# Kernel tuning notes

Hardware: AMD Instinct MI355X
Metric: run time of the kernel (lower is better)

The kernel has to match this reference:

```python
import jax, jax.numpy as jnp
import numpy as np
from jax import lax

MAX_T = 1.0
MAX_Z = float(np.e)  # exp(MAX_T)
BITS = 8


def weight_quantization(w):
    # tanh -> scale by max-abs (no grad through alpha) -> clamp -> round with STE
    w = jnp.tanh(w)
    alpha = lax.stop_gradient(jnp.max(jnp.abs(w)))
    q = 2 ** (BITS - 1) - 1
    w = jnp.clip(w / alpha, -1.0, 1.0) * q
    w = w + lax.stop_gradient(jnp.round(w) - w)
    return w * alpha / q


def t_linear_c(inp, W, max_spike_time):
    # inp: [B, L, Fin], W: [Fout, Fin] -> out: [B, L, Fout]
    idx = jnp.argsort(inp, axis=-1)                              # [B,L,Fin]
    s_inp = jnp.take_along_axis(inp, idx, axis=-1)[..., None]    # [B,L,Fin,1]
    w_sorted = W.T[idx]                                          # [B,L,Fin,Fout]
    w_sorted = weight_quantization(w_sorted)
    mul = s_inp * w_sorted
    w_sum = jnp.cumsum(w_sorted, axis=-2)
    iw_sum = jnp.cumsum(mul, axis=-2)
    out_all = iw_sum / jnp.clip(w_sum - 1.0, 1e-10, 1e10)
    o = jnp.where(w_sum < 1.0, max_spike_time, out_all)
    o = jnp.where(o < s_inp, max_spike_time, o)
    nxt = jnp.concatenate([s_inp[:, :, 1:, :], jnp.ones_like(s_inp[:, :, :1, :])], axis=2)
    o = jnp.where(o > nxt, max_spike_time, o)
    return jnp.min(o, axis=-2)


def t_linear(inp, W, max_spike_time):
    # inp: [B, Fin], W: [Fout, Fin] -> out: [B, Fout]
    idx = jnp.argsort(inp, axis=-1)
    s_inp = jnp.take_along_axis(inp, idx, axis=-1)[..., None]    # [B,Fin,1]
    w_sorted = W.T[idx]                                          # [B,Fin,Fout]
    mul = s_inp * w_sorted
    w_sum = jnp.cumsum(w_sorted, axis=1)
    iw_sum = jnp.cumsum(mul, axis=1)
    out_all = iw_sum / jnp.clip(w_sum - 1.0, 1e-10, 1e10)
    o = jnp.where(w_sum < 1.0, max_spike_time, out_all)
    o = jnp.where(o < s_inp, max_spike_time, o)
    nxt = jnp.concatenate([s_inp[:, 1:, :], jnp.ones_like(s_inp[:, :1, :])], axis=1)
    o = jnp.where(o >= nxt, max_spike_time, o)  # note: >= in t_Linear (vs > in t_Linear_c)
    return jnp.min(o, axis=1)


def unfold(x, k, p, s):
    # torch F.unfold: zero-pad, extract kxk patches; feature order (C, kh, kw)
    B, C, H, W = x.shape
    xp = jnp.pad(x, ((0, 0), (0, 0), (p, p), (p, p)))
    oh = (H + 2 * p - k) // s + 1
    ow = (W + 2 * p - k) // s + 1
    ri = (jnp.arange(oh) * s)[:, None] + jnp.arange(k)           # [oh,k]
    ci = (jnp.arange(ow) * s)[:, None] + jnp.arange(k)           # [ow,k]
    pt = xp[:, :, ri[:, None, :, None], ci[None, :, None, :]]    # [B,C,oh,ow,k,k]
    pt = pt.transpose(0, 2, 3, 1, 4, 5).reshape(B, oh * ow, C * k * k)
    return pt, oh, ow


def t_conv(x, W, k, pad, stride, max_spike_time):
    B = x.shape[0]
    patches, oh, ow = unfold(x, k, pad, stride)                  # [B,L,C*k*k]
    patches = jnp.where(patches < 0.1, max_spike_time, patches)
    out = t_linear_c(patches, W, max_spike_time)                 # [B,L,Cout]
    return out.transpose(0, 2, 1).reshape(B, W.shape[0], oh, ow)


def max_pool2(x):
    return lax.reduce_window(x, -jnp.inf, lax.max, (1, 1, 2, 2), (1, 1, 2, 2), 'VALID')


def min_pool3(x):
    # -MaxPool3x3(stride 2)(-ConstantPad2d(1, 1e5)(x))
    xp = jnp.pad(x, ((0, 0), (0, 0), (1, 1), (1, 1)), constant_values=1e5)
    return -lax.reduce_window(-xp, -jnp.inf, lax.max, (1, 1, 3, 3), (1, 1, 2, 2), 'VALID')


def setup_inputs() -> dict:
    key = jax.random.key(0)
    ks = jax.random.split(key, 8)
    B = 8
    inp = jax.random.normal(ks[0], (B, 1, 64, 64), dtype=jnp.float32)
    conv1_w = jax.random.normal(ks[1], (32, 1, 5, 5), dtype=jnp.float32) * (1.0 / 5.0)
    bn_g = jnp.ones((32,), jnp.float32)
    bn_b = jnp.zeros((32,), jnp.float32)
    bn_m = jnp.zeros((32,), jnp.float32)
    bn_v = jnp.ones((32,), jnp.float32)
    def uw(k, fout, fin):
        return jax.random.uniform(k, (fout, fin), jnp.float32, 0.0, 10.0 / fin)
    w2 = uw(ks[2], 32, 3 * 3 * 32)
    w3 = uw(ks[3], 32, 3 * 3 * 32)
    w4 = uw(ks[4], 64, 3 * 3 * 32)
    w5 = uw(ks[5], 64, 3 * 3 * 64)
    w_fc = uw(ks[6], 10, 8 * 8 * 64)
    return {"inp": inp, "conv1_w": conv1_w, "bn_g": bn_g, "bn_b": bn_b,
            "bn_m": bn_m, "bn_v": bn_v, "w2": w2, "w3": w3, "w4": w4,
            "w5": w5, "w_fc": w_fc}


def reference(inp, conv1_w, bn_g, bn_b, bn_m, bn_v, w2, w3, w4, w5, w_fc):
    x = lax.conv_general_dilated(inp, conv1_w, (1, 1), ((2, 2), (2, 2)),
                                 dimension_numbers=('NCHW', 'OIHW', 'NCHW'))
    x = (x - bn_m[None, :, None, None]) * (bn_g / jnp.sqrt(bn_v + 1e-5))[None, :, None, None] \
        + bn_b[None, :, None, None]
    x = jax.nn.relu(x)
    x = max_pool2(x)                       # [B,32,32,32]
    x = jnp.minimum(x, MAX_T)
    z1 = jnp.exp(x)
    z2 = t_conv(z1, w2, 3, 1, 2, MAX_Z)    # [B,32,16,16]
    z3 = t_conv(z2, w3, 3, 1, 1, MAX_Z)    # [B,32,16,16]
    z3c = z3 * min_pool3(z1)
    z4 = t_conv(z3c, w4, 3, 1, 2, MAX_Z * 2)  # [B,64,8,8]
    z5 = t_conv(z4, w5, 3, 1, 1, MAX_Z * 2)   # [B,64,8,8]
    pm = min_pool3(z3c)                       # [B,32,8,8]
    pm = jnp.concatenate([pm, pm], axis=1)    # [B,64,8,8]
    z5c = (z5 * pm).reshape(z5.shape[0], -1)  # [B,4096]
    return t_linear(z5c, w_fc, MAX_Z * 4)     # [B,10]
```

## Files before the change

kernel.cpp:

```cpp
#include <hip/hip_runtime.h>
#include <hip/hip_bf16.h>
#include <math.h>

#define E32 2.7182817459106445f

__device__ __forceinline__ unsigned long long packkey(float vf, int idx) {
  unsigned u = __float_as_uint(vf);
  u = (u & 0x80000000u) ? ~u : (u | 0x80000000u);
  return (((unsigned long long)u) << 32) | (unsigned)idx;
}
__device__ __forceinline__ float unpackval(unsigned long long k) {
  unsigned m = (unsigned)(k >> 32);
  m = (m & 0x80000000u) ? (m ^ 0x80000000u) : ~m;
  return __uint_as_float(m);
}

__global__ __launch_bounds__(256) void pre1_kernel(
    const float* __restrict__ w2, const float* __restrict__ w3,
    const float* __restrict__ w4, const float* __restrict__ w5,
    float* __restrict__ tanhbuf, float* __restrict__ partials,
    const float* __restrict__ inp, const float* __restrict__ w1,
    const float* __restrict__ g, const float* __restrict__ bb,
    const float* __restrict__ m, const float* __restrict__ vv,
    float* __restrict__ z1) {
  int blk = blockIdx.x;
  if (blk < 288) {
    const float* w; int base_blk, tbase;
    if (blk < 36)       { w = w2; base_blk = 0;   tbase = 0; }
    else if (blk < 72)  { w = w3; base_blk = 36;  tbase = 9216; }
    else if (blk < 144) { w = w4; base_blk = 72;  tbase = 18432; }
    else                { w = w5; base_blk = 144; tbase = 36864; }
    int i = (blk - base_blk) * 256 + threadIdx.x;
    float t = tanhf(w[i]);
    tanhbuf[tbase + i] = t;
    __shared__ float red[256];
    red[threadIdx.x] = fabsf(t);
    __syncthreads();
    for (int s = 128; s > 0; s >>= 1) {
      if (threadIdx.x < s) red[threadIdx.x] = fmaxf(red[threadIdx.x], red[threadIdx.x + s]);
      __syncthreads();
    }
    if (threadIdx.x == 0) partials[blk] = red[0];
    return;
  }
  int idx = (blk - 288) * 256 + threadIdx.x;
  if (idx >= 8 * 32 * 32 * 32) return;
  int x = idx & 31, y = (idx >> 5) & 31, c = (idx >> 10) & 31, b = idx >> 15;
  float scale = g[c] / sqrtf(vv[c] + 1e-5f);
  float bias = bb[c];
  float mean = m[c];
  float mx = -3.402823466e38f;
  for (int dy = 0; dy < 2; ++dy) {
    for (int dx = 0; dx < 2; ++dx) {
      int oy = 2 * y + dy, ox = 2 * x + dx;
      float acc = 0.0f;
      for (int kh = 0; kh < 5; ++kh) {
        int r = oy + kh - 2;
        if (r < 0 || r >= 64) continue;
        for (int kw = 0; kw < 5; ++kw) {
          int cc2 = ox + kw - 2;
          if (cc2 < 0 || cc2 >= 64) continue;
          acc += w1[c * 25 + kh * 5 + kw] * inp[(b * 64 + r) * 64 + cc2];
        }
      }
      float xs = (acc - mean) * scale + bias;
      xs = fmaxf(xs, 0.0f);
      mx = fmaxf(mx, xs);
    }
  }
  mx = fminf(mx, 1.0f);
  z1[idx] = (mx == 1.0f) ? E32 : expf(mx);
}

__global__ __launch_bounds__(256) void pre2_kernel(
    const float* __restrict__ tanhbuf, const float* __restrict__ partials,
    float* __restrict__ q2, float* __restrict__ q3,
    float* __restrict__ q4, float* __restrict__ q5,
    const float* __restrict__ wfc, float* __restrict__ wfcT,
    const float* __restrict__ z1, float* __restrict__ m1) {
  int blk = blockIdx.x;
  if (blk >= 448) {
    int idx = (blk - 448) * 256 + threadIdx.x;
    if (idx >= 65536) return;
    int OH = 16;
    int j = idx % OH, i = (idx / OH) % OH, bc = idx / (OH * OH);
    float mn = 100000.0f;
    for (int di = 0; di < 3; ++di) {
      int r = 2 * i - 1 + di;
      if (r < 0 || r >= 32) continue;
      for (int dj = 0; dj < 3; ++dj) {
        int cc = 2 * j - 1 + dj;
        if (cc < 0 || cc >= 32) continue;
        mn = fminf(mn, z1[bc * 1024 + r * 32 + cc]);
      }
    }
    m1[idx] = mn;
    return;
  }
  if (blk >= 288) {
    int o = (blk - 288) * 256 + threadIdx.x;
    if (o < 40960) {
      int n = o / 10, f = o % 10;
      wfcT[o] = wfc[f * 4096 + n];
    }
    return;
  }
  float* dst; int base_blk, tbase, pb0, pb1, F, N;
  if (blk < 36)       { dst = q2; base_blk = 0;   tbase = 0;     pb0 = 0;   pb1 = 36;  F = 32; N = 288; }
  else if (blk < 72)  { dst = q3; base_blk = 36;  tbase = 9216;  pb0 = 36;  pb1 = 72;  F = 32; N = 288; }
  else if (blk < 144) { dst = q4; base_blk = 72;  tbase = 18432; pb0 = 72;  pb1 = 144; F = 64; N = 288; }
  else                { dst = q5; base_blk = 144; tbase = 36864; pb0 = 144; pb1 = 288; F = 64; N = 576; }
  __shared__ float red[256];
  float mx = 0.0f;
  for (int j = pb0 + threadIdx.x; j < pb1; j += 256) mx = fmaxf(mx, partials[j]);
  red[threadIdx.x] = mx;
  __syncthreads();
  for (int s = 128; s > 0; s >>= 1) {
    if (threadIdx.x < s) red[threadIdx.x] = fmaxf(red[threadIdx.x], red[threadIdx.x + s]);
    __syncthreads();
  }
  float a = red[0];
  int i = (blk - base_blk) * 256 + threadIdx.x;
  float t = tanhbuf[tbase + i];
  int f = i / N, n = i % N;
  float r = fminf(fmaxf(t / a, -1.0f), 1.0f) * 127.0f;
  dst[n * F + f] = rintf(r) * a / 127.0f;
}

template <int CIN, int F, int S, int HIN, bool MUL>
__device__ __forceinline__ void tconv_body(
    const float* __restrict__ in, const float* __restrict__ in2,
    const float* __restrict__ wqt, float* __restrict__ out, float MST,
    int patch, int tid) {
  constexpr int N = CIN * 9;
  constexpr int NP = (N <= 512) ? 512 : 1024;
  constexpr int KP = NP / 512;
  constexpr int OH = (HIN - 1) / S + 1;
  constexpr int P = OH * OH;
  constexpr int T = 512;
  constexpr int NCH = N / 32;

  __shared__ __align__(16) unsigned long long pk[NP];
  __shared__ float sval[N + 1];
  __shared__ unsigned short sidx[N];
  __shared__ float wbuf[2][32 * F];
  __shared__ float wc[NCH][F];
  __shared__ float iwc[NCH][F];
  __shared__ float pmin[F * NCH];

  int b = patch / P, p = patch % P;
  int ph = p / OH, pw = p % OH;

  for (int n = tid; n < NP; n += T) {
    if (n < N) {
      int c = n / 9, kk = n % 9, kh = kk / 3, kw = kk % 3;
      int r = ph * S + kh - 1, cc = pw * S + kw - 1;
      float v = 0.0f;
      if (r >= 0 && r < HIN && cc >= 0 && cc < HIN) {
        int q = ((b * CIN + c) * HIN + r) * HIN + cc;
        v = MUL ? __fmul_rn(in[q], in2[q]) : in[q];
      }
      pk[n] = packkey((v < 0.1f) ? MST : v, n);
    } else {
      pk[n] = ~0ull;
    }
  }
  if (tid == 0) sval[N] = 1.0f;
  __syncthreads();

  if constexpr (KP == 1) {
    unsigned long long k0 = pk[tid];
    __syncthreads();
    for (int lk = 1; lk <= 9; ++lk) {
      for (int lj = lk - 1; lj >= 0; --lj) {
        int j = 1 << lj;
        bool up = ((tid >> lk) & 1) == 0;
        bool wmin = (((tid & j) == 0) == up);
        unsigned long long o;
        if (lj >= 6) {
          pk[tid] = k0;
          __syncthreads();
          o = pk[tid ^ j];
          __syncthreads();
        } else {
          o = __shfl_xor(k0, j, 64);
        }
        k0 = wmin ? (k0 < o ? k0 : o) : (k0 > o ? k0 : o);
      }
    }
    if (tid < N) {
      sval[tid] = unpackval(k0);
      sidx[tid] = (unsigned short)(k0 & 0xffffull);
    }
  } else {
    unsigned long long k0 = pk[2 * tid], k1 = pk[2 * tid + 1];
    __syncthreads();
    for (int lk = 1; lk <= 10; ++lk) {
      for (int lj = lk - 1; lj >= 0; --lj) {
        bool up = ((tid >> (lk - 1)) & 1) == 0;
        if (lj == 0) {
          if ((k0 > k1) == up) { unsigned long long t2 = k0; k0 = k1; k1 = t2; }
        } else {
          int tj = 1 << (lj - 1);
          bool wmin = (((tid & tj) == 0) == up);
          unsigned long long o0, o1;
          if (lj >= 7) {
            pk[tid] = k0; pk[512 + tid] = k1;
            __syncthreads();
            o0 = pk[tid ^ tj]; o1 = pk[512 + (tid ^ tj)];
            __syncthreads();
          } else {
            o0 = __shfl_xor(k0, tj, 64);
            o1 = __shfl_xor(k1, tj, 64);
          }
          k0 = wmin ? (k0 < o0 ? k0 : o0) : (k0 > o0 ? k0 : o0);
          k1 = wmin ? (k1 < o1 ? k1 : o1) : (k1 > o1 ? k1 : o1);
        }
      }
    }
    int i0 = tid * 2;
    if (i0 < N) {
      sval[i0] = unpackval(k0);
      sidx[i0] = (unsigned short)(k0 & 0xffffull);
    }
    if (i0 + 1 < N) {
      sval[i0 + 1] = unpackval(k1);
      sidx[i0 + 1] = (unsigned short)(k1 & 0xffffull);
    }
  }
  __syncthreads();

  for (int t = tid; t < 32 * F; t += T) {
    int q = t / F, f = t % F;
    wbuf[0][t] = wqt[(int)sidx[q] * F + f];
  }
  __syncthreads();

  float wsum = 0.0f, iwsum = 0.0f;
  for (int c = 0; c < NCH; ++c) {
    if (tid >= 64 && c + 1 < NCH) {
      int i0n = (c + 1) * 32;
      float* nb = wbuf[(c + 1) & 1];
      for (int t = tid - 64; t < 32 * F; t += (T - 64)) {
        int q = t / F, f = t % F;
        nb[t] = wqt[(int)sidx[i0n + q] * F + f];
      }
    }
    if (tid < F) {
      const float* wb = wbuf[c & 1];
      wc[c][tid] = wsum;
      iwc[c][tid] = iwsum;
      int i0 = c * 32;
#pragma unroll
      for (int q0 = 0; q0 < 32; q0 += 8) {
        float w8[8], s8[8];
#pragma unroll
        for (int r = 0; r < 8; ++r) {
          w8[r] = wb[(q0 + r) * F + tid];
          s8[r] = sval[i0 + q0 + r];
        }
#pragma unroll
        for (int r = 0; r < 8; ++r) {
          wsum = __fadd_rn(wsum, w8[r]);
          iwsum = __fadd_rn(iwsum, __fmul_rn(s8[r], w8[r]));
        }
      }
    }
    __syncthreads();
  }

  for (int task = tid; task < NCH * F; task += T) {
    int c = task / F, f = task % F;
    float ws = wc[c][f], iws = iwc[c][f], omin = 3.402823466e38f;
    int i0 = c * 32;
#pragma unroll
    for (int q0 = 0; q0 < 32; q0 += 8) {
      float wv8[8], sv8[8], nv8[8];
#pragma unroll
      for (int r = 0; r < 8; ++r) {
        int i = i0 + q0 + r;
        wv8[r] = wqt[(int)sidx[i] * F + f];
        sv8[r] = sval[i];
        nv8[r] = sval[i + 1];
      }
#pragma unroll
      for (int r = 0; r < 8; ++r) {
        ws = __fadd_rn(ws, wv8[r]);
        iws = __fadd_rn(iws, __fmul_rn(sv8[r], wv8[r]));
        float den = fminf(fmaxf(__fadd_rn(ws, -1.0f), 1e-10f), 1e10f);
        float oa = iws / den;
        float o = (ws < 1.0f) ? MST : oa;
        o = (o < sv8[r]) ? MST : o;
        o = (o > nv8[r]) ? MST : o;
        omin = fminf(omin, o);
      }
    }
    pmin[f * NCH + c] = omin;
  }
  __syncthreads();

  if (tid < F) {
    float m2 = pmin[tid * NCH];
#pragma unroll
    for (int c = 1; c < NCH; ++c) m2 = fminf(m2, pmin[tid * NCH + c]);
    out[(b * F + tid) * P + p] = m2;
  }
}

template <int CIN, int F, int S, int HIN, bool MUL>
__global__ __launch_bounds__(512, 1) void tconv_kernel(
    const float* __restrict__ in, const float* __restrict__ in2,
    const float* __restrict__ wqt, float* __restrict__ out, float MST) {
  tconv_body<CIN, F, S, HIN, MUL>(in, in2, wqt, out, MST, blockIdx.x, threadIdx.x);
}

__global__ __launch_bounds__(512, 1) void t4f_kernel(
    const float* __restrict__ z3, const float* __restrict__ m1,
    const float* __restrict__ wq4, float* __restrict__ z4,
    float* __restrict__ m3, float MST) {
  int blk = blockIdx.x;
  if (blk < 512) {
    tconv_body<32, 64, 2, 16, true>(z3, m1, wq4, z4, MST, blk, threadIdx.x);
    return;
  }
  int idx = (blk - 512) * 512 + threadIdx.x;
  if (idx >= 16384) return;
  int OH = 8;
  int j = idx % OH, i = (idx / OH) % OH, bc = idx / (OH * OH);
  float mn = 100000.0f;
  for (int di = 0; di < 3; ++di) {
    int r = 2 * i - 1 + di;
    if (r < 0 || r >= 16) continue;
    for (int dj = 0; dj < 3; ++dj) {
      int cc = 2 * j - 1 + dj;
      if (cc < 0 || cc >= 16) continue;
      int q = bc * 256 + r * 16 + cc;
      mn = fminf(mn, __fmul_rn(z3[q], m1[q]));
    }
  }
  m3[idx] = mn;
}

template <int LK, int LJ>
__device__ __forceinline__ void bpass(unsigned long long (&k)[8],
                                      unsigned long long* keys,
                                      int tid, int lane) {
  if constexpr (LJ >= 9) {
    constexpr int pm = 1 << (LJ - 3);
#pragma unroll
    for (int m = 0; m < 8; ++m) keys[m * 512 + tid] = k[m];
    __syncthreads();
    bool lower = ((tid & pm) == 0);
    bool up = (((tid >> (LK - 3)) & 1) == 0);
    bool wmin = (lower == up);
#pragma unroll
    for (int m = 0; m < 8; ++m) {
      unsigned long long o = keys[m * 512 + (tid ^ pm)];
      unsigned long long mine = k[m];
      k[m] = wmin ? (mine < o ? mine : o) : (mine > o ? mine : o);
    }
    __syncthreads();
  } else if constexpr (LJ >= 3) {
    constexpr int lm = 1 << (LJ - 3);
    bool lower = ((lane & lm) == 0);
    bool up = (((tid >> (LK - 3)) & 1) == 0);
    bool wmin = (lower == up);
#pragma unroll
    for (int m = 0; m < 8; ++m) {
      unsigned long long o = __shfl_xor(k[m], lm, 64);
      unsigned long long mine = k[m];
      k[m] = wmin ? (mine < o ? mine : o) : (mine > o ? mine : o);
    }
  } else {
    constexpr int j = 1 << LJ;
#pragma unroll
    for (int m = 0; m < 8; ++m) {
      if ((m & j) == 0) {
        int i = (tid << 3) + m;
        bool up = (((i >> LK) & 1) == 0);
        unsigned long long a = k[m], c2 = k[m | j];
        if ((a > c2) == up) { k[m] = c2; k[m | j] = a; }
      }
    }
  }
}

template <int LK, int LJ>
__device__ __forceinline__ void bpasses(unsigned long long (&k)[8],
                                        unsigned long long* keys,
                                        int tid, int lane) {
  bpass<LK, LJ>(k, keys, tid, lane);
  if constexpr (LJ > 0) bpasses<LK, LJ - 1>(k, keys, tid, lane);
}

template <int LK>
__device__ __forceinline__ void bstages(unsigned long long (&k)[8],
                                        unsigned long long* keys,
                                        int tid, int lane) {
  bpasses<LK, LK - 1>(k, keys, tid, lane);
  if constexpr (LK < 12) bstages<LK + 1>(k, keys, tid, lane);
}

__global__ __launch_bounds__(512, 1) void fc_sort_kernel(
    const float* __restrict__ z5, const float* __restrict__ m3,
    float* __restrict__ svalG, unsigned short* __restrict__ sidxG) {
  __shared__ __align__(16) unsigned long long keys[4096];
  int b = blockIdx.x, tid = threadIdx.x, lane = tid & 63;

  unsigned long long k[8];
  {
    int c = tid >> 3, p0 = (tid << 3) & 63;
    const float4* z4p = (const float4*)(z5 + (b * 64 + c) * 64 + p0);
    const float4* m4p = (const float4*)(m3 + (b * 32 + (c & 31)) * 64 + p0);
    float4 za = z4p[0], zb = z4p[1], ma = m4p[0], mb = m4p[1];
    int n0 = tid << 3;
    k[0] = packkey(__fmul_rn(za.x, ma.x), n0 + 0);
    k[1] = packkey(__fmul_rn(za.y, ma.y), n0 + 1);
    k[2] = packkey(__fmul_rn(za.z, ma.z), n0 + 2);
    k[3] = packkey(__fmul_rn(za.w, ma.w), n0 + 3);
    k[4] = packkey(__fmul_rn(zb.x, mb.x), n0 + 4);
    k[5] = packkey(__fmul_rn(zb.y, mb.y), n0 + 5);
    k[6] = packkey(__fmul_rn(zb.z, mb.z), n0 + 6);
    k[7] = packkey(__fmul_rn(zb.w, mb.w), n0 + 7);
  }

  bstages<1>(k, keys, tid, lane);

  {
    float4 v0, v1;
    v0.x = unpackval(k[0]); v0.y = unpackval(k[1]);
    v0.z = unpackval(k[2]); v0.w = unpackval(k[3]);
    v1.x = unpackval(k[4]); v1.y = unpackval(k[5]);
    v1.z = unpackval(k[6]); v1.w = unpackval(k[7]);
    float* svalRow = svalG + b * 4104;
    ((float4*)svalRow)[tid * 2] = v0;
    ((float4*)svalRow)[tid * 2 + 1] = v1;
    ushort si[8];
#pragma unroll
    for (int m = 0; m < 8; ++m) si[m] = (unsigned short)(k[m] & 0xffffull);
    ((ulong2*)(sidxG + b * 4096))[tid] = *(ulong2*)si;
    if (tid == 0) svalRow[4096] = 1.0f;
  }
}

__global__ __launch_bounds__(512, 1) void fc_scan2_kernel(
    const float* __restrict__ svalG, const unsigned short* __restrict__ sidxG,
    const float* __restrict__ wfcT, float* __restrict__ out) {
  constexpr int NN = 4096;
  __shared__ __align__(16) float sval[NN + 1];
  __shared__ __align__(16) float pairs[NN * 2];
  __shared__ float wc[128], iwc[128];
  __shared__ float pmin[128];

  int blk = blockIdx.x;
  int b = blk / 10, f = blk % 10;
  int tid = threadIdx.x;
  const float* svalRow = svalG + b * 4104;

  for (int t = tid; t < 1024; t += 512)
    ((float4*)sval)[t] = ((const float4*)svalRow)[t];
  if (tid == 0) sval[NN] = svalRow[4096];

  ushort si[8];
  *(ulong2*)si = ((const ulong2*)(sidxG + b * 4096))[tid];
  float wv[8];
#pragma unroll
  for (int u = 0; u < 8; ++u) wv[u] = wfcT[(int)si[u] * 10 + f];
  __syncthreads();

  {
    int n0 = tid * 8;
    float4 pw[4];
#pragma unroll
    for (int u = 0; u < 4; ++u) {
      float wa = wv[2 * u], wb2 = wv[2 * u + 1];
      pw[u].x = wa;
      pw[u].y = __fmul_rn(sval[n0 + 2 * u], wa);
      pw[u].z = wb2;
      pw[u].w = __fmul_rn(sval[n0 + 2 * u + 1], wb2);
    }
#pragma unroll
    for (int u = 0; u < 4; ++u) ((float4*)pairs)[tid * 4 + u] = pw[u];
  }
  __syncthreads();

  if (tid == 0) {
    float wsum = 0.0f, iwsum = 0.0f;
    float4 A[16], B[16];
    auto LD_A = [&](int c) {
      const float4* p4 = (const float4*)pairs + c * 16;
#pragma unroll
      for (int q = 0; q < 16; ++q) A[q] = p4[q];
    };
    auto LD_B = [&](int c) {
      const float4* p4 = (const float4*)pairs + c * 16;
#pragma unroll
      for (int q = 0; q < 16; ++q) B[q] = p4[q];
    };
    auto ACC_A = [&]() {
#pragma unroll
      for (int q = 0; q < 16; ++q) {
        wsum = __fadd_rn(wsum, A[q].x); iwsum = __fadd_rn(iwsum, A[q].y);
        wsum = __fadd_rn(wsum, A[q].z); iwsum = __fadd_rn(iwsum, A[q].w);
      }
    };
    auto ACC_B = [&]() {
#pragma unroll
      for (int q = 0; q < 16; ++q) {
        wsum = __fadd_rn(wsum, B[q].x); iwsum = __fadd_rn(iwsum, B[q].y);
        wsum = __fadd_rn(wsum, B[q].z); iwsum = __fadd_rn(iwsum, B[q].w);
      }
    };
    LD_A(0);
    for (int c = 0; c < 128; c += 2) {
      wc[c] = wsum; iwc[c] = iwsum;
      if (c + 1 < 128) LD_B(c + 1);
      ACC_A();
      wc[c + 1] = wsum; iwc[c + 1] = iwsum;
      if (c + 2 < 128) LD_A(c + 2);
      ACC_B();
    }
  }
  __syncthreads();

  const float MST = 4.0f * E32;
  if (tid < 128) {
    float ws = wc[tid], iws = iwc[tid], omin = 3.402823466e38f;
    int i0 = tid * 32;
    for (int q0 = 0; q0 < 32; q0 += 8) {
      float w8[8], m8[8], sv8[8], nv8[8];
#pragma unroll
      for (int r = 0; r < 8; ++r) {
        int i = i0 + q0 + r;
        w8[r] = pairs[2 * i];
        m8[r] = pairs[2 * i + 1];
        sv8[r] = sval[i];
        nv8[r] = sval[i + 1];
      }
#pragma unroll
      for (int r = 0; r < 8; ++r) {
        ws = __fadd_rn(ws, w8[r]);
        iws = __fadd_rn(iws, m8[r]);
        float den = fminf(fmaxf(__fadd_rn(ws, -1.0f), 1e-10f), 1e10f);
        float oa = iws / den;
        float o = (ws < 1.0f) ? MST : oa;
        o = (o < sv8[r]) ? MST : o;
        o = (o >= nv8[r]) ? MST : o;
        omin = fminf(omin, o);
      }
    }
    pmin[tid] = omin;
  }
  __syncthreads();

  if (tid == 0) {
    float m = pmin[0];
    for (int c = 1; c < 128; ++c) m = fminf(m, pmin[c]);
    out[b * 10 + f] = m;
  }
}

extern "C" void kernel_launch(void* const* d_in, const int* in_sizes, int n_in,
                              void* d_out, int out_size, void* d_ws, size_t ws_size,
                              hipStream_t stream) {
  const float* inp   = (const float*)d_in[0];
  const float* w1    = (const float*)d_in[1];
  const float* bn_g  = (const float*)d_in[2];
  const float* bn_b  = (const float*)d_in[3];
  const float* bn_m  = (const float*)d_in[4];
  const float* bn_v  = (const float*)d_in[5];
  const float* w2    = (const float*)d_in[6];
  const float* w3    = (const float*)d_in[7];
  const float* w4    = (const float*)d_in[8];
  const float* w5    = (const float*)d_in[9];
  const float* wfc   = (const float*)d_in[10];
  float* out = (float*)d_out;

  float* ws = (float*)d_ws;
  float* wq2 = ws + 16;
  float* wq3 = wq2 + 9216;
  float* wq4 = wq3 + 9216;
  float* wq5 = wq4 + 18432;
  float* z1  = wq5 + 36864;
  float* m1  = z1 + 262144;
  float* z2  = m1 + 65536;
  float* z3  = z2 + 65536;
  float* m3  = z3 + 65536;
  float* z4  = m3 + 16384;
  float* z5  = z4 + 32768;
  float* tanhbuf  = z5 + 32768;
  float* partials = tanhbuf + 73728;
  float* wfcT = partials + 512;
  float* svalG = wfcT + 40960;
  unsigned short* sidxG = (unsigned short*)(svalG + 32832);

  pre1_kernel<<<1312, 256, 0, stream>>>(w2, w3, w4, w5, tanhbuf, partials,
                                        inp, w1, bn_g, bn_b, bn_m, bn_v, z1);
  pre2_kernel<<<704, 256, 0, stream>>>(tanhbuf, partials, wq2, wq3, wq4, wq5,
                                       wfc, wfcT, z1, m1);

  tconv_kernel<32, 32, 2, 32, false><<<8 * 256, 512, 0, stream>>>(z1, nullptr, wq2, z2, E32);
  tconv_kernel<32, 32, 1, 16, false><<<8 * 256, 512, 0, stream>>>(z2, nullptr, wq3, z3, E32);
  t4f_kernel<<<544, 512, 0, stream>>>(z3, m1, wq4, z4, m3, 2.0f * E32);
  tconv_kernel<64, 64, 1, 8, false><<<8 * 64, 512, 0, stream>>>(z4, nullptr, wq5, z5, 2.0f * E32);

  fc_sort_kernel<<<8, 512, 0, stream>>>(z5, m3, svalG, sidxG);
  fc_scan2_kernel<<<80, 512, 0, stream>>>(svalG, sidxG, wfcT, out);
}
```

Measured before the change: 224.8 us.

## Double-buffer bitonic exchange, widen weight staging chunks, alias shared memory

The bitonic sort's shared-memory exchange now alternates between two buffers, which drops the second barrier in each cross-wave step. The weight gather/prefix-sum pipeline stages 96 rows per chunk instead of 32, so it needs fewer block-wide barriers. The sort keys, weight staging buffer and pmin now share one aliased LDS region to hold down shared-memory use. The larger staging buffer could still raise LDS footprint and lower occupancy, and the aliasing relies on correct barrier ordering between phases.

```diff
diff --git a/kernel.cpp b/kernel.cpp
--- a/kernel.cpp
+++ b/kernel.cpp
@@ -139,14 +139,25 @@
   constexpr int P = OH * OH;
   constexpr int T = 512;
   constexpr int NCH = N / 32;
-
-  __shared__ __align__(16) unsigned long long pk[NP];
+  constexpr int SC = 96;
+  constexpr int NSC = N / SC;
+  static_assert(N % SC == 0, "SC must divide N");
+
+  constexpr int AB_SORT = 2 * NP * 8;
+  constexpr int AB_WBUF = 2 * SC * F * 4;
+  constexpr int AB_PMIN = F * NCH * 4;
+  constexpr int AB1 = (AB_SORT > AB_WBUF) ? AB_SORT : AB_WBUF;
+  constexpr int AB = (AB1 > AB_PMIN) ? AB1 : AB_PMIN;
+
+  __shared__ __align__(16) unsigned char alias_mem[AB];
+  unsigned long long* pk  = (unsigned long long*)alias_mem;
+  unsigned long long* pkB = pk + NP;
+  float* wbuf = (float*)alias_mem;
+  float* pmin = (float*)alias_mem;
   __shared__ float sval[N + 1];
   __shared__ unsigned short sidx[N];
-  __shared__ float wbuf[2][32 * F];
   __shared__ float wc[NCH][F];
   __shared__ float iwc[NCH][F];
-  __shared__ float pmin[F * NCH];
 
   int b = patch / P, p = patch % P;
   int ph = p / OH, pw = p % OH;
@@ -168,6 +179,7 @@
   if (tid == 0) sval[N] = 1.0f;
   __syncthreads();
 
+  int par = 0;
   if constexpr (KP == 1) {
     unsigned long long k0 = pk[tid];
     __syncthreads();
@@ -178,10 +190,11 @@
         bool wmin = (((tid & j) == 0) == up);
         unsigned long long o;
         if (lj >= 6) {
-          pk[tid] = k0;
+          unsigned long long* bk = par ? pkB : pk;
+          bk[tid] = k0;
           __syncthreads();
-          o = pk[tid ^ j];
-          __syncthreads();
+          o = bk[tid ^ j];
+          par ^= 1;
         } else {
           o = __shfl_xor(k0, j, 64);
         }
@@ -205,10 +218,11 @@
           bool wmin = (((tid & tj) == 0) == up);
           unsigned long long o0, o1;
           if (lj >= 7) {
-            pk[tid] = k0; pk[512 + tid] = k1;
+            unsigned long long* bk = par ? pkB : pk;
+            bk[tid] = k0; bk[512 + tid] = k1;
             __syncthreads();
-            o0 = pk[tid ^ tj]; o1 = pk[512 + (tid ^ tj)];
-            __syncthreads();
+            o0 = bk[tid ^ tj]; o1 = bk[512 + (tid ^ tj)];
+            par ^= 1;
           } else {
             o0 = __shfl_xor(k0, tj, 64);
             o1 = __shfl_xor(k1, tj, 64);
@@ -230,39 +244,41 @@
   }
   __syncthreads();
 
-  for (int t = tid; t < 32 * F; t += T) {
+  for (int t = tid; t < SC * F; t += T) {
     int q = t / F, f = t % F;
-    wbuf[0][t] = wqt[(int)sidx[q] * F + f];
+    wbuf[t] = wqt[(int)sidx[q] * F + f];
   }
   __syncthreads();
 
   float wsum = 0.0f, iwsum = 0.0f;
-  for (int c = 0; c < NCH; ++c) {
-    if (tid >= 64 && c + 1 < NCH) {
-      int i0n = (c + 1) * 32;
-      float* nb = wbuf[(c + 1) & 1];
-      for (int t = tid - 64; t < 32 * F; t += (T - 64)) {
+  for (int c = 0; c < NSC; ++c) {
+    if (tid >= 64 && c + 1 < NSC) {
+      int i0n = (c + 1) * SC;
+      float* nb = wbuf + ((c + 1) & 1) * (SC * F);
+      for (int t = tid - 64; t < SC * F; t += (T - 64)) {
         int q = t / F, f = t % F;
         nb[t] = wqt[(int)sidx[i0n + q] * F + f];
       }
     }
     if (tid < F) {
-      const float* wb = wbuf[c & 1];
-      wc[c][tid] = wsum;
-      iwc[c][tid] = iwsum;
-      int i0 = c * 32;
-#pragma unroll
-      for (int q0 = 0; q0 < 32; q0 += 8) {
-        float w8[8], s8[8];
-#pragma unroll
-        for (int r = 0; r < 8; ++r) {
-          w8[r] = wb[(q0 + r) * F + tid];
-          s8[r] = sval[i0 + q0 + r];
-        }
-#pragma unroll
-        for (int r = 0; r < 8; ++r) {
-          wsum = __fadd_rn(wsum, w8[r]);
-          iwsum = __fadd_rn(iwsum, __fmul_rn(s8[r], w8[r]));
+      const float* wb = wbuf + (c & 1) * (SC * F);
+      int base = c * SC;
+      for (int q0 = 0; q0 < SC; q0 += 32) {
+        wc[(base + q0) >> 5][tid] = wsum;
+        iwc[(base + q0) >> 5][tid] = iwsum;
+#pragma unroll
+        for (int qq = 0; qq < 32; qq += 8) {
+          float w8[8], s8[8];
+#pragma unroll
+          for (int r = 0; r < 8; ++r) {
+            w8[r] = wb[(q0 + qq + r) * F + tid];
+            s8[r] = sval[base + q0 + qq + r];
+          }
+#pragma unroll
+          for (int r = 0; r < 8; ++r) {
+            wsum = __fadd_rn(wsum, w8[r]);
+            iwsum = __fadd_rn(iwsum, __fmul_rn(s8[r], w8[r]));
+          }
         }
       }
     }
```

Result: no change. 225.3 us (+0.2%).
